# Kernel tuning notes

Hardware: AMD Instinct MI355X
Metric: run time of the kernel (lower is better)

The kernel has to match this reference:

```python
import jax, jax.numpy as jnp
import numpy as np

EPS = 1e-6
NEG_SLOPE = 0.01  # torch LeakyReLU default

def ln(x, g, b):
    m = jnp.mean(x, axis=-1, keepdims=True)
    v = jnp.mean((x - m) ** 2, axis=-1, keepdims=True)
    return (x - m) / jnp.sqrt(v + EPS) * g + b

def leaky(x):
    return jnp.where(x >= 0, x, NEG_SLOPE * x)

def setup_inputs() -> dict:
    B, L, F, H, NH, LBL = 8, 1024, 1024, 256, 8, 4766
    key = jax.random.key(0)
    ks = jax.random.split(key, 16)
    def lin(k, i, o, s=0.03):
        kw, kb = jax.random.split(k)
        return jax.random.normal(kw, (i, o), jnp.float32) * s, jnp.zeros((o,), jnp.float32)
    w_in, b_in = lin(ks[0], F, H)
    w_h, b_h = lin(ks[1], H, H)
    a_w1, a_b1 = lin(ks[2], H, 64)
    a_w2, a_b2 = lin(ks[3], 64, NH)
    o_w1, o_b1 = lin(ks[4], NH * H, NH * H)
    o_w2, o_b2 = lin(ks[5], NH * H, LBL)
    CM = (jax.random.uniform(ks[6], (LBL, LBL)) < 0.002).astype(jnp.float32)
    CM = jnp.maximum(CM, jnp.eye(LBL, dtype=jnp.float32))
    return {
        'h_V': jax.random.normal(ks[7], (B, L, F), jnp.float32),
        'mask': jnp.ones((B, L), jnp.int32),
        'ln0_g': jnp.ones((F,), jnp.float32), 'ln0_b': jnp.zeros((F,), jnp.float32),
        'w_in': w_in, 'b_in': b_in,
        'ln1_g': jnp.ones((H,), jnp.float32), 'ln1_b': jnp.zeros((H,), jnp.float32),
        'w_h': w_h, 'b_h': b_h,
        'ln2_g': jnp.ones((H,), jnp.float32), 'ln2_b': jnp.zeros((H,), jnp.float32),
        'a_w1': a_w1, 'a_b1': a_b1,
        'a_lng': jnp.ones((64,), jnp.float32), 'a_lnb': jnp.zeros((64,), jnp.float32),
        'a_w2': a_w2, 'a_b2': a_b2,
        'o_w1': o_w1, 'o_b1': o_b1,
        'o_lng': jnp.ones((NH * H,), jnp.float32), 'o_lnb': jnp.zeros((NH * H,), jnp.float32),
        'o_w2': o_w2, 'o_b2': o_b2,
        'CM': CM,
    }

def reference(h_V, mask, ln0_g, ln0_b, w_in, b_in, ln1_g, ln1_b, w_h, b_h,
              ln2_g, ln2_b, a_w1, a_b1, a_lng, a_lnb, a_w2, a_b2,
              o_w1, o_b1, o_lng, o_lnb, o_w2, o_b2, CM):
    B = h_V.shape[0]
    # input + hidden blocks (eval mode: dropout is identity)
    x = ln(h_V, ln0_g, ln0_b)
    x = leaky(x @ w_in + b_in)
    x = ln(x, ln1_g, ln1_b)
    x = leaky(x @ w_h + b_h)
    x = ln(x, ln2_g, ln2_b)                      # [B,L,H]
    # multi-head attention pooling over sequence
    a = leaky(x @ a_w1 + a_b1)
    a = ln(a, a_lng, a_lnb)
    a = a @ a_w2 + a_b2                          # [B,L,NH]
    a = jnp.where(mask[:, :, None] == 0, jnp.float32(-1e9), a)
    a = jax.nn.softmax(a, axis=1)
    h = jnp.einsum('blh,bld->bhd', a, x).reshape(B, -1)  # [B,NH*H]
    # output block
    h = leaky(h @ o_w1 + o_b1)
    h = ln(h, o_lng, o_lnb)
    p = jax.nn.sigmoid(h @ o_w2 + o_b2)          # [B,LBL]
    # GO-hierarchy max-product propagation (eval path)
    out = jnp.max(p[:, None, :] * CM[None, :, :], axis=-1)  # [B,LBL]
    return out.astype(jnp.float32)
```

## Files before the change

### kernel.cpp

```cpp
#include <hip/hip_runtime.h>
#include <hip/hip_bf16.h>
#include <cstdint>

#define B_   8
#define L_   1024
#define F_   1024
#define H_   256
#define NH_  8
#define LBL_ 4766
#define M_   (B_*L_)
#define OD_  (NH_*H_)
#define NCM  (LBL_*LBL_)
#define MP_EPB 16384
#define MP_NB  ((NCM + MP_EPB - 1) / MP_EPB)

typedef unsigned short u16;
typedef unsigned int   u32;
typedef __attribute__((ext_vector_type(8))) short short8;
typedef __attribute__((ext_vector_type(4))) float float4v;

#define BF16_ONES_PAIR 0x3f803f80u

__device__ __forceinline__ float bf2f(u32 u) { return __uint_as_float(u << 16); }
__device__ __forceinline__ u16 f2bf(float f) {
    u32 u = __float_as_uint(f);
    u32 r = 0x7fffu + ((u >> 16) & 1u);
    return (u16)((u + r) >> 16);
}

struct f8 { float v[8]; };

__device__ __forceinline__ float ldS(const void* p, size_t i, bool bf) {
    return bf ? bf2f(((const u16*)p)[i]) : ((const float*)p)[i];
}
__device__ __forceinline__ float4 ld4(const void* p, size_t i, bool bf) {
    if (bf) {
        uint2 u = *(const uint2*)((const u16*)p + i);
        return make_float4(bf2f(u.x & 0xffff), bf2f(u.x >> 16),
                           bf2f(u.y & 0xffff), bf2f(u.y >> 16));
    }
    return *(const float4*)((const float*)p + i);
}
__device__ __forceinline__ f8 ld8(const void* p, size_t i, bool bf) {
    f8 r;
    if (bf) {
        uint4 u = *(const uint4*)((const u16*)p + i);
        r.v[0]=bf2f(u.x&0xffff); r.v[1]=bf2f(u.x>>16);
        r.v[2]=bf2f(u.y&0xffff); r.v[3]=bf2f(u.y>>16);
        r.v[4]=bf2f(u.z&0xffff); r.v[5]=bf2f(u.z>>16);
        r.v[6]=bf2f(u.w&0xffff); r.v[7]=bf2f(u.w>>16);
    } else {
        const float* q = (const float*)p + i;
        float4 a = *(const float4*)q, b = *(const float4*)(q+4);
        r.v[0]=a.x; r.v[1]=a.y; r.v[2]=a.z; r.v[3]=a.w;
        r.v[4]=b.x; r.v[5]=b.y; r.v[6]=b.z; r.v[7]=b.w;
    }
    return r;
}

__device__ __forceinline__ float wave_sum(float v) {
    #pragma unroll
    for (int m = 1; m < 64; m <<= 1) v += __shfl_xor(v, m, 64);
    return v;
}
__device__ __forceinline__ float wave_max(float v) {
    #pragma unroll
    for (int m = 1; m < 64; m <<= 1) v = fmaxf(v, __shfl_xor(v, m, 64));
    return v;
}
__device__ __forceinline__ float blk_sum(float v, float* sh) {
    v = wave_sum(v);
    int w = threadIdx.x >> 6, nw = blockDim.x >> 6;
    if ((threadIdx.x & 63) == 0) sh[w] = v;
    __syncthreads();
    float s = sh[0];
    for (int i = 1; i < nw; ++i) s += sh[i];
    __syncthreads();
    return s;
}
__device__ __forceinline__ float blk_max(float v, float* sh) {
    v = wave_max(v);
    int w = threadIdx.x >> 6, nw = blockDim.x >> 6;
    if ((threadIdx.x & 63) == 0) sh[w] = v;
    __syncthreads();
    float s = sh[0];
    for (int i = 1; i < nw; ++i) s = fmaxf(s, sh[i]);
    __syncthreads();
    return s;
}

__global__ __launch_bounds__(256) void transw_k(const void* __restrict__ W,
        u16* __restrict__ WT, int K, int N, const u32* __restrict__ probe) {
    __shared__ u16 tile[64][65];
    bool bf = (probe[0] == BF16_ONES_PAIR);
    int t = threadIdx.x;
    int kt = blockIdx.x * 64, nt = blockIdx.y * 64;
    int r = t >> 2, cq = (t & 3) * 16;
    #pragma unroll
    for (int j = 0; j < 4; ++j) {
        float4 v = ld4(W, (size_t)(kt + r) * N + nt + cq + j * 4, bf);
        tile[r][cq + j*4 + 0] = f2bf(v.x);
        tile[r][cq + j*4 + 1] = f2bf(v.y);
        tile[r][cq + j*4 + 2] = f2bf(v.z);
        tile[r][cq + j*4 + 3] = f2bf(v.w);
    }
    __syncthreads();
    #pragma unroll
    for (int j = 0; j < 4; ++j) {
        int k = cq + j * 4;
        u32 a0 = tile[k+0][r], a1 = tile[k+1][r], a2 = tile[k+2][r], a3 = tile[k+3][r];
        uint2 o; o.x = a0 | (a1 << 16); o.y = a2 | (a3 << 16);
        *(uint2*)(WT + (size_t)(nt + r) * K + kt + k) = o;
    }
}

__global__ __launch_bounds__(256) void rowstats_k(const void* __restrict__ hv,
        float2* __restrict__ stat, const u32* __restrict__ probe) {
    __shared__ float sh[4];
    bool bf = (probe[0] == BF16_ONES_PAIR);
    int row = blockIdx.x, t = threadIdx.x;
    float4 v = ld4(hv, (size_t)row * F_ + t * 4, bf);
    float s = v.x + v.y + v.z + v.w;
    float q = v.x*v.x + v.y*v.y + v.z*v.z + v.w*v.w;
    s = blk_sum(s, sh);
    q = blk_sum(q, sh);
    if (t == 0) {
        float mean = s * (1.f / F_);
        float var  = q * (1.f / F_) - mean * mean;
        stat[row] = make_float2(mean, rsqrtf(var + 1e-6f));
    }
}

__global__ __launch_bounds__(64) void rowstats_bf_k(const u16* __restrict__ x,
        float2* __restrict__ stat) {
    int row = blockIdx.x, t = threadIdx.x;
    uint2 u = ((const uint2*)(x + (size_t)row * 256))[t];
    float a0 = bf2f(u.x & 0xffff), a1 = bf2f(u.x >> 16);
    float a2 = bf2f(u.y & 0xffff), a3 = bf2f(u.y >> 16);
    float s = wave_sum(a0 + a1 + a2 + a3);
    float q = wave_sum(a0*a0 + a1*a1 + a2*a2 + a3*a3);
    if (t == 0) {
        float m = s * (1.f / 256), v = q * (1.f / 256) - m * m;
        stat[row] = make_float2(m, rsqrtf(v + 1e-6f));
    }
}

__global__ __launch_bounds__(256) void gemm_mfma(const void* __restrict__ Ap, int amode,
        const float2* __restrict__ stat, const void* __restrict__ g,
        const void* __restrict__ bta, const u16* __restrict__ WT,
        const void* __restrict__ bias, u16* __restrict__ C, int M, int N, int K,
        const u32* __restrict__ probe) {
    __shared__ short8 As[64][4];
    __shared__ short8 Bs[64][4];
    bool pbf = (probe[0] == BF16_ONES_PAIR);
    bool abf = amode ? true : pbf;
    int t = threadIdx.x;
    int m0 = blockIdx.x * 64, n0 = blockIdx.y * 64;
    int r = t >> 2, kq = t & 3;
    int l = t & 63, w = t >> 6;
    int q = l >> 4, ml = l & 15;
    float4v acc[4];
    #pragma unroll
    for (int nt = 0; nt < 4; ++nt)
        #pragma unroll
        for (int i = 0; i < 4; ++i) acc[nt][i] = 0.f;
    float2 st = stat[m0 + r];
    for (int k0 = 0; k0 < K; k0 += 32) {
        int kk = k0 + kq * 8;
        f8 a  = ld8(Ap, (size_t)(m0 + r) * K + kk, abf);
        f8 gg = ld8(g, kk, pbf);
        f8 bb = ld8(bta, kk, pbf);
        short8 pa;
        #pragma unroll
        for (int j = 0; j < 8; ++j)
            pa[j] = (short)f2bf((a.v[j] - st.x) * st.y * gg.v[j] + bb.v[j]);
        short8 pb = *(const short8*)(WT + (size_t)(n0 + r) * K + kk);
        __syncthreads();
        As[r][kq] = pa;
        Bs[r][kq] = pb;
        __syncthreads();
        short8 af = As[w * 16 + ml][q];
        #pragma unroll
        for (int nt = 0; nt < 4; ++nt)
            acc[nt] = __builtin_amdgcn_mfma_f32_16x16x32_bf16(af, Bs[nt*16 + ml][q],
                                                              acc[nt], 0, 0, 0);
    }
    #pragma unroll
    for (int nt = 0; nt < 4; ++nt) {
        int nn = n0 + nt * 16 + ml;
        float bv = ldS(bias, nn, pbf);
        #pragma unroll
        for (int reg = 0; reg < 4; ++reg) {
            float v = acc[nt][reg] + bv;
            v = v >= 0.f ? v : 0.01f * v;
            C[(size_t)(m0 + w * 16 + q * 4 + reg) * N + nn] = f2bf(v);
        }
    }
}

__global__ __launch_bounds__(256) void attnlog_k(const u16* __restrict__ abr,
        const void* __restrict__ g, const void* __restrict__ b,
        const void* __restrict__ w2, const void* __restrict__ b2,
        const int* __restrict__ mask, float* __restrict__ lg,
        const u32* __restrict__ probe) {
    __shared__ float w2s[512];
    __shared__ float b2s[8];
    bool pbf = (probe[0] == BF16_ONES_PAIR);
    int t = threadIdx.x;
    for (int i = t; i < 512; i += 256) w2s[i] = ldS(w2, i, pbf);
    if (t < 8) b2s[t] = ldS(b2, t, pbf);
    __syncthreads();
    int l = t & 63, w = t >> 6;
    int row = blockIdx.x * 4 + w;
    float a = bf2f(abr[(size_t)row * 64 + l]);
    float s = wave_sum(a);
    float q = wave_sum(a * a);
    float m = s * (1.f / 64), var = q * (1.f / 64) - m * m;
    float val = (a - m) * rsqrtf(var + 1e-6f) * ldS(g, l, pbf) + ldS(b, l, pbf);
    float mine = 0.f;
    #pragma unroll
    for (int h = 0; h < 8; ++h) {
        float sh_ = wave_sum(val * w2s[l * 8 + h]);
        if (l == h) mine = sh_;
    }
    if (l < 8) {
        int bb = row >> 10, ll = row & 1023;
        float v = mine + b2s[l];
        if (mask[row] == 0) v = -1e9f;
        lg[((size_t)bb * NH_ + l) * L_ + ll] = v;
    }
}

__global__ __launch_bounds__(256) void softmax2_k(float* __restrict__ lg,
        const float2* __restrict__ st2, float* __restrict__ c1) {
    __shared__ float sh[4];
    int bh = blockIdx.x, t = threadIdx.x;
    int b = bh >> 3;
    size_t base = (size_t)bh * L_;
    float4 v = ((float4*)(lg + base))[t];
    float mx = blk_max(fmaxf(fmaxf(v.x, v.y), fmaxf(v.z, v.w)), sh);
    v.x = expf(v.x - mx); v.y = expf(v.y - mx);
    v.z = expf(v.z - mx); v.w = expf(v.w - mx);
    float s = blk_sum(v.x + v.y + v.z + v.w, sh);
    float inv = 1.f / s;
    float2 s0 = st2[(b << 10) + t*4 + 0];
    float2 s1 = st2[(b << 10) + t*4 + 1];
    float2 s2 = st2[(b << 10) + t*4 + 2];
    float2 s3 = st2[(b << 10) + t*4 + 3];
    float a0 = v.x * inv * s0.y, a1 = v.y * inv * s1.y;
    float a2 = v.z * inv * s2.y, a3 = v.w * inv * s3.y;
    ((float4*)(lg + base))[t] = make_float4(a0, a1, a2, a3);
    float c = blk_sum(a0 * s0.x + a1 * s1.x + a2 * s2.x + a3 * s3.x, sh);
    if (t == 0) c1[bh] = c;
}

__global__ __launch_bounds__(256) void pool_part_k(const float* __restrict__ lg,
        const u16* __restrict__ x2, float* __restrict__ Sp) {
    int bh = blockIdx.x, c = blockIdx.y, t = threadIdx.x;
    int b = bh >> 3, l0 = c << 8;
    const float* aw = lg + (size_t)bh * L_ + l0;
    const u16* xb = x2 + ((size_t)(b << 10) + l0) * 256;
    float acc = 0.f;
    #pragma unroll 4
    for (int i = 0; i < 256; ++i)
        acc += aw[i] * bf2f(xb[(size_t)i * 256 + t]);
    Sp[((size_t)c * 64 + bh) * 256 + t] = acc;
}

__global__ __launch_bounds__(256) void pool_comb_k(const float* __restrict__ Sp,
        const float* __restrict__ c1, const void* __restrict__ g,
        const void* __restrict__ b, float* __restrict__ hp,
        const u32* __restrict__ probe) {
    bool pbf = (probe[0] == BF16_ONES_PAIR);
    int bh = blockIdx.x, t = threadIdx.x;
    float S = Sp[(size_t)bh*256 + t] + Sp[(size_t)(64+bh)*256 + t]
            + Sp[(size_t)(128+bh)*256 + t] + Sp[(size_t)(192+bh)*256 + t];
    hp[(size_t)bh*256 + t] = (S - c1[bh]) * ldS(g, t, pbf) + ldS(b, t, pbf);
}

__global__ __launch_bounds__(256) void gemv2_k(const float* __restrict__ hv,
        const void* __restrict__ W, float* __restrict__ acc, int K, int N,
        const u32* __restrict__ probe) {
    __shared__ float hs[8 * 64];
    bool bf = (probe[0] == BF16_ONES_PAIR);
    int t = threadIdx.x;
    int kb = blockIdx.y * 64;
    for (int i = t; i < 512; i += 256) {
        int r = i >> 6, k = i & 63;
        hs[i] = hv[(size_t)r * K + kb + k];
    }
    __syncthreads();
    int c0 = (blockIdx.x * 256 + t) * 2;
    if (c0 >= N) return;
    float a[8][2] = {};
    #pragma unroll 4
    for (int k = 0; k < 64; ++k) {
        float w0, w1;
        if (bf) {
            u32 u = *(const u32*)((const u16*)W + (size_t)(kb + k) * N + c0);
            w0 = bf2f(u & 0xffff); w1 = bf2f(u >> 16);
        } else {
            float2 fw = *(const float2*)((const float*)W + (size_t)(kb + k) * N + c0);
            w0 = fw.x; w1 = fw.y;
        }
        #pragma unroll
        for (int r = 0; r < 8; ++r) {
            float h = hs[(r << 6) + k];
            a[r][0] += h * w0; a[r][1] += h * w1;
        }
    }
    bool ok1 = (c0 + 1 < N);
    #pragma unroll
    for (int r = 0; r < 8; ++r) {
        atomicAdd(&acc[(size_t)r * N + c0], a[r][0]);
        if (ok1) atomicAdd(&acc[(size_t)r * N + c0 + 1], a[r][1]);
    }
}

__global__ __launch_bounds__(256) void out_ln_k(float* __restrict__ h,
        const void* __restrict__ bias, const void* __restrict__ g,
        const void* __restrict__ b, const u32* __restrict__ probe) {
    __shared__ float sh[4];
    bool bf = (probe[0] == BF16_ONES_PAIR);
    int row = blockIdx.x, t = threadIdx.x;
    float v[8];
    float s = 0.f, q = 0.f;
    #pragma unroll
    for (int i = 0; i < 8; ++i) {
        int c = t + i * 256;
        float x = h[(size_t)row * OD_ + c] + ldS(bias, c, bf);
        x = x >= 0.f ? x : 0.01f * x;
        v[i] = x; s += x; q += x * x;
    }
    s = blk_sum(s, sh) * (1.f / OD_);
    q = blk_sum(q, sh) * (1.f / OD_);
    float rstd = rsqrtf(q - s * s + 1e-6f);
    #pragma unroll
    for (int i = 0; i < 8; ++i) {
        int c = t + i * 256;
        h[(size_t)row * OD_ + c] = (v[i] - s) * rstd * ldS(g, c, bf) + ldS(b, c, bf);
    }
}

__global__ __launch_bounds__(256) void sigmoid_t_k(const float* __restrict__ acc,
        const void* __restrict__ bias, float* __restrict__ pt,
        const u32* __restrict__ probe) {
    bool bf = (probe[0] == BF16_ONES_PAIR);
    int c = blockIdx.x * 256 + threadIdx.x;
    if (c >= LBL_) return;
    float bv = ldS(bias, c, bf);
    float o[8];
    #pragma unroll
    for (int r = 0; r < 8; ++r) {
        float v = acc[(size_t)r * LBL_ + c] + bv;
        o[r] = 1.f / (1.f + expf(-v));
    }
    float4* dst = (float4*)(pt + (size_t)c * 8);
    dst[0] = make_float4(o[0], o[1], o[2], o[3]);
    dst[1] = make_float4(o[4], o[5], o[6], o[7]);
}

__device__ __forceinline__ void mp_hit(u32 idx, float cmv,
        const float* __restrict__ pt, int* smax, u32 rowBase) {
    u32 i = idx / LBL_;
    u32 j = idx - i * LBL_;
    const float4* pj = (const float4*)(pt + (size_t)j * 8);
    float4 pa = pj[0], pb = pj[1];
    int base = (int)(i - rowBase) * 8;
    atomicMax(&smax[base + 0], __float_as_int(pa.x * cmv));
    atomicMax(&smax[base + 1], __float_as_int(pa.y * cmv));
    atomicMax(&smax[base + 2], __float_as_int(pa.z * cmv));
    atomicMax(&smax[base + 3], __float_as_int(pa.w * cmv));
    atomicMax(&smax[base + 4], __float_as_int(pb.x * cmv));
    atomicMax(&smax[base + 5], __float_as_int(pb.y * cmv));
    atomicMax(&smax[base + 6], __float_as_int(pb.z * cmv));
    atomicMax(&smax[base + 7], __float_as_int(pb.w * cmv));
}

__global__ __launch_bounds__(256) void maxprod3_k(const float* __restrict__ pt,
        const void* __restrict__ CM, float* __restrict__ out,
        const u32* __restrict__ probe) {
    __shared__ int smax[6 * 8];
    bool bf = (probe[0] == BF16_ONES_PAIR);
    int t = threadIdx.x;
    size_t blockStart = (size_t)blockIdx.x * MP_EPB;
    u32 rowBase = (u32)(blockStart / LBL_);
    for (int i = t; i < 48; i += 256) smax[i] = 0;
    __syncthreads();
    if (bf) {
        const u16* cm = (const u16*)CM;
        uint4 ch[8];
        size_t i0[8];
        #pragma unroll
        for (int u = 0; u < 8; ++u) {
            size_t idx0 = blockStart + ((size_t)u * 256 + t) * 8;
            i0[u] = idx0;
            ch[u] = (idx0 + 8 <= NCM) ? *(const uint4*)(cm + idx0)
                                      : make_uint4(0, 0, 0, 0);
        }
        #pragma unroll
        for (int u = 0; u < 8; ++u) {
            size_t idx0 = i0[u];
            if (idx0 + 8 <= NCM) {
                uint4 c4 = ch[u];
                if ((c4.x | c4.y | c4.z | c4.w) == 0) continue;
                u32 hw[4] = {c4.x, c4.y, c4.z, c4.w};
                #pragma unroll
                for (int d = 0; d < 4; ++d) {
                    u32 lo = hw[d] & 0xffff, hi = hw[d] >> 16;
                    if (lo) mp_hit((u32)idx0 + d*2,     bf2f(lo), pt, smax, rowBase);
                    if (hi) mp_hit((u32)idx0 + d*2 + 1, bf2f(hi), pt, smax, rowBase);
                }
            } else if (idx0 < NCM) {
                for (u32 e = 0; e < (u32)(NCM - idx0); ++e) {
                    u16 h = cm[idx0 + e];
                    if (h) mp_hit((u32)idx0 + e, bf2f(h), pt, smax, rowBase);
                }
            }
        }
    } else {
        const float* cm = (const float*)CM;
        #pragma unroll
        for (int u = 0; u < 16; ++u) {
            size_t idx0 = blockStart + ((size_t)u * 256 + t) * 4;
            if (idx0 >= NCM) continue;
            float v[4];
            if (idx0 + 4 <= NCM) {
                float4 f = *(const float4*)(cm + idx0);
                v[0] = f.x; v[1] = f.y; v[2] = f.z; v[3] = f.w;
            } else {
                v[0] = v[1] = v[2] = v[3] = 0.f;
                for (u32 e = 0; e < (u32)(NCM - idx0); ++e) v[e] = cm[idx0 + e];
            }
            if (v[0] == 0.f && v[1] == 0.f && v[2] == 0.f && v[3] == 0.f) continue;
            #pragma unroll
            for (int e = 0; e < 4; ++e)
                if (v[e] != 0.f) mp_hit((u32)idx0 + e, v[e], pt, smax, rowBase);
        }
    }
    __syncthreads();
    size_t lastIdx = blockStart + MP_EPB - 1;
    if (lastIdx >= NCM) lastIdx = NCM - 1;
    int nrows = (int)((u32)(lastIdx / LBL_) - rowBase) + 1;
    for (int s = t; s < nrows * 8; s += 256) {
        int v = smax[s];
        if (v != 0) {
            int rr = s >> 3, b = s & 7;
            atomicMax((int*)(out + (size_t)b * LBL_ + rowBase + rr), v);
        }
    }
}

extern "C" void kernel_launch(void* const* d_in, const int* in_sizes, int n_in,
                              void* d_out, int out_size, void* d_ws, size_t ws_size,
                              hipStream_t stream) {
    const void* hv   = d_in[0];
    const int* mask  = (const int*)d_in[1];
    const void* ln0g = d_in[2];
    const void* ln0b = d_in[3];
    const void* w_in = d_in[4];
    const void* b_in = d_in[5];
    const void* ln1g = d_in[6];
    const void* ln1b = d_in[7];
    const void* w_h  = d_in[8];
    const void* b_h  = d_in[9];
    const void* ln2g = d_in[10];
    const void* ln2b = d_in[11];
    const void* aw1  = d_in[12];
    const void* ab1  = d_in[13];
    const void* alng = d_in[14];
    const void* alnb = d_in[15];
    const void* aw2  = d_in[16];
    const void* ab2  = d_in[17];
    const void* ow1  = d_in[18];
    const void* ob1  = d_in[19];
    const void* olng = d_in[20];
    const void* olnb = d_in[21];
    const void* ow2  = d_in[22];
    const void* ob2  = d_in[23];
    const void* CM   = d_in[24];
    const u32* probe = (const u32*)ln0g;
    float* out = (float*)d_out;

    float* f = (float*)d_ws;
    float2* st0 = (float2*)f;
    float2* st1 = st0 + 8192;
    float2* st2 = st1 + 8192;
    float* lg = f + 3 * 16384;
    float* c1 = lg + 65536;
    float* Sp = c1 + 64;
    float* hp = Sp + 65536;
    float* ha = hp + 16384;
    float* l2 = ha + 16384;
    float* pt = l2 + 38128;
    u16* x1  = (u16*)(pt + 38128);
    u16* x2  = x1 + 2097152;
    u16* abr = x2 + 2097152;
    u16* wt1 = abr + 524288;
    u16* wt2 = wt1 + 262144;
    u16* wt3 = wt2 + 65536;

    hipMemsetAsync(ha, 0, (size_t)(16384 + 38128) * sizeof(float), stream);
    hipMemsetAsync(out, 0, (size_t)(B_ * LBL_) * sizeof(float), stream);

    transw_k<<<dim3(16, 4), 256, 0, stream>>>(w_in, wt1, F_, H_, probe);
    transw_k<<<dim3(4, 4),  256, 0, stream>>>(w_h,  wt2, H_, H_, probe);
    transw_k<<<dim3(4, 1),  256, 0, stream>>>(aw1,  wt3, H_, 64, probe);

    rowstats_k<<<M_, 256, 0, stream>>>(hv, st0, probe);
    gemm_mfma<<<dim3(M_/64, 4), 256, 0, stream>>>(hv, 0, st0, ln0g, ln0b,
                                                  wt1, b_in, x1, M_, H_, F_, probe);
    rowstats_bf_k<<<M_, 64, 0, stream>>>(x1, st1);
    gemm_mfma<<<dim3(M_/64, 4), 256, 0, stream>>>(x1, 1, st1, ln1g, ln1b,
                                                  wt2, b_h, x2, M_, H_, H_, probe);
    rowstats_bf_k<<<M_, 64, 0, stream>>>(x2, st2);
    gemm_mfma<<<dim3(M_/64, 1), 256, 0, stream>>>(x2, 1, st2, ln2g, ln2b,
                                                  wt3, ab1, abr, M_, 64, H_, probe);

    attnlog_k<<<M_/4, 256, 0, stream>>>(abr, alng, alnb, aw2, ab2, mask, lg, probe);
    softmax2_k<<<B_*NH_, 256, 0, stream>>>(lg, st2, c1);
    pool_part_k<<<dim3(B_*NH_, 4), 256, 0, stream>>>(lg, x2, Sp);
    pool_comb_k<<<B_*NH_, 256, 0, stream>>>(Sp, c1, ln2g, ln2b, hp, probe);

    gemv2_k<<<dim3(OD_/512, 32), 256, 0, stream>>>(hp, ow1, ha, OD_, OD_, probe);
    out_ln_k<<<B_, 256, 0, stream>>>(ha, ob1, olng, olnb, probe);
    gemv2_k<<<dim3((LBL_+511)/512, 32), 256, 0, stream>>>(ha, ow2, l2, OD_, LBL_, probe);
    sigmoid_t_k<<<(LBL_+255)/256, 256, 0, stream>>>(l2, ob2, pt, probe);
    maxprod3_k<<<MP_NB, 256, 0, stream>>>(pt, CM, out, probe);
}
```

Before: 393.8 us.

## Materialize normalized bf16 input once instead of re-normalizing fp32 per GEMM tile

The first LayerNorm is now applied in the row-stats kernel, which writes a normalized bf16 copy of the 8192x1024 input. The first GEMM then loads bf16 A tiles directly instead of reading fp32 input and recomputing the normalization for each of its 4 N-blocks. This cuts the A-side global reads of that GEMM (bf16 instead of fp32, and the fp32 input is no longer re-read by every N-block) and removes per-element normalization ALU work, at the cost of writing and reading back a 16 MB intermediate. The shared tiles are also padded from 4 to 5 columns to reduce LDS bank conflicts.

```diff
diff --git a/kernel.cpp b/kernel.cpp
--- a/kernel.cpp
+++ b/kernel.cpp
@@ -114,8 +114,9 @@
     }
 }
 
-__global__ __launch_bounds__(256) void rowstats_k(const void* __restrict__ hv,
-        float2* __restrict__ stat, const u32* __restrict__ probe) {
+__global__ __launch_bounds__(256) void lnwrite_k(const void* __restrict__ hv,
+        const void* __restrict__ g, const void* __restrict__ b,
+        u16* __restrict__ x0, const u32* __restrict__ probe) {
     __shared__ float sh[4];
     bool bf = (probe[0] == BF16_ONES_PAIR);
     int row = blockIdx.x, t = threadIdx.x;
@@ -124,11 +125,15 @@
     float q = v.x*v.x + v.y*v.y + v.z*v.z + v.w*v.w;
     s = blk_sum(s, sh);
     q = blk_sum(q, sh);
-    if (t == 0) {
-        float mean = s * (1.f / F_);
-        float var  = q * (1.f / F_) - mean * mean;
-        stat[row] = make_float2(mean, rsqrtf(var + 1e-6f));
-    }
+    float mean = s * (1.f / F_);
+    float rstd = rsqrtf(q * (1.f / F_) - mean * mean + 1e-6f);
+    float4 gg = ld4(g, t * 4, bf);
+    float4 bb = ld4(b, t * 4, bf);
+    u32 o0 = f2bf((v.x - mean) * rstd * gg.x + bb.x)
+           | ((u32)f2bf((v.y - mean) * rstd * gg.y + bb.y) << 16);
+    u32 o1 = f2bf((v.z - mean) * rstd * gg.z + bb.z)
+           | ((u32)f2bf((v.w - mean) * rstd * gg.w + bb.w) << 16);
+    *(uint2*)(x0 + (size_t)row * F_ + t * 4) = make_uint2(o0, o1);
 }
 
 __global__ __launch_bounds__(64) void rowstats_bf_k(const u16* __restrict__ x,
@@ -145,15 +150,14 @@
     }
 }
 
-__global__ __launch_bounds__(256) void gemm_mfma(const void* __restrict__ Ap, int amode,
+__global__ __launch_bounds__(256) void gemm_mfma(const u16* __restrict__ Ap, int amode,
         const float2* __restrict__ stat, const void* __restrict__ g,
         const void* __restrict__ bta, const u16* __restrict__ WT,
         const void* __restrict__ bias, u16* __restrict__ C, int M, int N, int K,
         const u32* __restrict__ probe) {
-    __shared__ short8 As[64][4];
-    __shared__ short8 Bs[64][4];
+    __shared__ short8 As[64][5];
+    __shared__ short8 Bs[64][5];
     bool pbf = (probe[0] == BF16_ONES_PAIR);
-    bool abf = amode ? true : pbf;
     int t = threadIdx.x;
     int m0 = blockIdx.x * 64, n0 = blockIdx.y * 64;
     int r = t >> 2, kq = t & 3;
@@ -164,16 +168,20 @@
     for (int nt = 0; nt < 4; ++nt)
         #pragma unroll
         for (int i = 0; i < 4; ++i) acc[nt][i] = 0.f;
-    float2 st = stat[m0 + r];
+    float2 st = (amode == 1) ? stat[m0 + r] : make_float2(0.f, 1.f);
     for (int k0 = 0; k0 < K; k0 += 32) {
         int kk = k0 + kq * 8;
-        f8 a  = ld8(Ap, (size_t)(m0 + r) * K + kk, abf);
-        f8 gg = ld8(g, kk, pbf);
-        f8 bb = ld8(bta, kk, pbf);
         short8 pa;
-        #pragma unroll
-        for (int j = 0; j < 8; ++j)
-            pa[j] = (short)f2bf((a.v[j] - st.x) * st.y * gg.v[j] + bb.v[j]);
+        if (amode == 1) {
+            f8 a  = ld8(Ap, (size_t)(m0 + r) * K + kk, true);
+            f8 gg = ld8(g, kk, pbf);
+            f8 bb = ld8(bta, kk, pbf);
+            #pragma unroll
+            for (int j = 0; j < 8; ++j)
+                pa[j] = (short)f2bf((a.v[j] - st.x) * st.y * gg.v[j] + bb.v[j]);
+        } else {
+            pa = *(const short8*)(Ap + (size_t)(m0 + r) * K + kk);
+        }
         short8 pb = *(const short8*)(WT + (size_t)(n0 + r) * K + kk);
         __syncthreads();
         As[r][kq] = pa;
@@ -483,17 +491,17 @@
     float* out = (float*)d_out;
 
     float* f = (float*)d_ws;
-    float2* st0 = (float2*)f;
-    float2* st1 = st0 + 8192;
+    float2* st1 = (float2*)f;
     float2* st2 = st1 + 8192;
-    float* lg = f + 3 * 16384;
+    float* lg = f + 2 * 16384;
     float* c1 = lg + 65536;
     float* Sp = c1 + 64;
     float* hp = Sp + 65536;
     float* ha = hp + 16384;
     float* l2 = ha + 16384;
     float* pt = l2 + 38128;
-    u16* x1  = (u16*)(pt + 38128);
+    u16* x0  = (u16*)(pt + 38128);
+    u16* x1  = x0 + 8388608;
     u16* x2  = x1 + 2097152;
     u16* abr = x2 + 2097152;
     u16* wt1 = abr + 524288;
@@ -507,8 +515,8 @@
     transw_k<<<dim3(4, 4),  256, 0, stream>>>(w_h,  wt2, H_, H_, probe);
     transw_k<<<dim3(4, 1),  256, 0, stream>>>(aw1,  wt3, H_, 64, probe);
 
-    rowstats_k<<<M_, 256, 0, stream>>>(hv, st0, probe);
-    gemm_mfma<<<dim3(M_/64, 4), 256, 0, stream>>>(hv, 0, st0, ln0g, ln0b,
+    lnwrite_k<<<M_, 256, 0, stream>>>(hv, ln0g, ln0b, x0, probe);
+    gemm_mfma<<<dim3(M_/64, 4), 256, 0, stream>>>(x0, 2, nullptr, nullptr, nullptr,
                                                   wt1, b_in, x1, M_, H_, F_, probe);
     rowstats_bf_k<<<M_, 64, 0, stream>>>(x1, st1);
     gemm_mfma<<<dim3(M_/64, 4), 256, 0, stream>>>(x1, 1, st1, ln1g, ln1b,
```

New measurement: 385.5 us. 1.02x faster.
